# Performance work log

Hardware: AMD Instinct MI355X
Metric: run time of the kernel (lower is better)

## Reference

```python
import jax, jax.numpy as jnp
import numpy as np

EMBED = 2048
HEADS = 16
B, T = 4, 2048


def setup_inputs() -> dict:
    key = jax.random.key(0)
    ks = jax.random.split(key, 8)
    s = 1.0 / np.sqrt(EMBED)
    return {
        "k": jax.random.normal(ks[0], (B, T, EMBED), dtype=jnp.float32),
        "q": jax.random.normal(ks[1], (B, T, EMBED), dtype=jnp.float32),
        "v": jax.random.normal(ks[2], (B, T, EMBED), dtype=jnp.float32),
        "Wk": jax.random.uniform(ks[3], (EMBED, EMBED), jnp.float32, -s, s),
        "Wq": jax.random.uniform(ks[4], (EMBED, EMBED), jnp.float32, -s, s),
        "Wv": jax.random.uniform(ks[5], (EMBED, EMBED), jnp.float32, -s, s),
        "Wo": jax.random.uniform(ks[6], (EMBED, EMBED), jnp.float32, -s, s),
        "bo": jax.random.uniform(ks[7], (EMBED,), jnp.float32, -s, s),
    }


def _split_heads(x):
    b, t, e = x.shape
    # 'b t (h n) -> b h t n'
    return x.reshape(b, t, HEADS, e // HEADS).transpose(0, 2, 1, 3)


def reference(k, q, v, Wk, Wq, Wv, Wo, bo):
    keys = _split_heads(k @ Wk.T)      # [b,h,t,n]
    queries = _split_heads(q @ Wq.T)
    values = _split_heads(v @ Wv.T)
    head_dim = queries.shape[-1]
    scale = 1.0 / jnp.sqrt(jnp.asarray(head_dim, queries.dtype))
    att = jnp.einsum('bhqn,bhkn->bhqk', queries, keys) * scale
    att = jax.nn.softmax(att, axis=-1)
    out = jnp.einsum('bhqk,bhkn->bhqn', att, values)  # [b,h,t,n]
    b, h, t, n = out.shape
    out = out.transpose(0, 2, 1, 3).reshape(b, t, h * n)  # 'b h t n -> b t (h n)'
    return out @ Wo.T + bo
```

## Files before the change

### kernel.cpp

```cpp
#include <hip/hip_runtime.h>


typedef __attribute__((ext_vector_type(4))) float f32x4;
typedef __attribute__((ext_vector_type(2))) float f32x2;
typedef __attribute__((ext_vector_type(8))) __bf16 bf16x8;
typedef __attribute__((ext_vector_type(4))) unsigned int u32x4;
typedef __attribute__((ext_vector_type(2))) unsigned int u32x2;

#define DEVI static __device__ __forceinline__

#define SCQ 0.12751721769f

DEVI unsigned short f2bf(float f) {
  union { float f; unsigned u; } x; x.f = f;
  unsigned u = x.u;
  return (unsigned short)((u + 0x7fffu + ((u >> 16) & 1u)) >> 16);
}
DEVI unsigned int pack2(float lo, float hi) {
  return (unsigned int)f2bf(lo) | ((unsigned int)f2bf(hi) << 16);
}
DEVI u32x4 pack8(const f32x4 a, const f32x4 b) {
  u32x4 r;
  r[0] = pack2(a[0], a[1]); r[1] = pack2(a[2], a[3]);
  r[2] = pack2(b[0], b[1]); r[3] = pack2(b[2], b[3]);
  return r;
}
DEVI void gload16(const unsigned short* g, unsigned short* l) {
  __builtin_amdgcn_global_load_lds(
      (const __attribute__((address_space(1))) unsigned int*)g,
      (__attribute__((address_space(3))) unsigned int*)l, 16, 0, 0);
}

template <int CTRL> DEVI float dppf(float x) {
  return __builtin_bit_cast(float, __builtin_amdgcn_update_dpp(
      __builtin_bit_cast(int, x), __builtin_bit_cast(int, x), CTRL, 0xF, 0xF, true));
}
DEVI float rowmax16(float x) {
  x = fmaxf(x, dppf<0x121>(x));
  x = fmaxf(x, dppf<0x122>(x));
  x = fmaxf(x, dppf<0x124>(x));
  x = fmaxf(x, dppf<0x128>(x));
  return x;
}
DEVI float rowsum16(float x) {
  x += dppf<0x121>(x);
  x += dppf<0x122>(x);
  x += dppf<0x124>(x);
  x += dppf<0x128>(x);
  return x;
}

__global__ __launch_bounds__(256) void convA(
    const float* __restrict__ q, const float* __restrict__ k,
    const float* __restrict__ v, unsigned short* __restrict__ dst)
{
  const int z = blockIdx.z;
  const float* src = z == 0 ? q : (z == 1 ? k : v);
  const float scl = z == 0 ? SCQ : 1.0f;
  unsigned short* d = dst + (size_t)z * 16777216;
  size_t i = ((size_t)blockIdx.x * 256 + threadIdx.x) * 8;
  f32x4 a = *(const f32x4*)(src + i) * scl;
  f32x4 b = *(const f32x4*)(src + i + 4) * scl;
  *(u32x4*)(d + i) = pack8(a, b);
}

__global__ __launch_bounds__(256) void convW(
    const float* __restrict__ w0, const float* __restrict__ w1,
    const float* __restrict__ w2, const float* __restrict__ w3,
    unsigned short* __restrict__ dst)
{
  const int z = blockIdx.z;
  const float* src = z == 0 ? w0 : (z == 1 ? w1 : (z == 2 ? w2 : w3));
  unsigned short* d = dst + (size_t)z * 4194304;
  size_t i = ((size_t)blockIdx.x * 256 + threadIdx.x) * 8;
  f32x4 a = *(const f32x4*)(src + i);
  f32x4 b = *(const f32x4*)(src + i + 4);
  *(u32x4*)(d + i) = pack8(a, b);
}

#define STG1(gp, lp, tile) gload16((gp) + (size_t)(tile) * 32, (lp));
#define LDA8(bufoff) { \
    _Pragma("unroll") for (int m = 0; m < 8; m++) \
      a[m] = *(const bf16x8*)(As + (bufoff) + aoff[m]); }
#define LDB2(bufoff, n0) { \
    b0 = *(const bf16x8*)(Bs + (bufoff) + boff[n0]); \
    b1 = *(const bf16x8*)(Bs + (bufoff) + boff[(n0) + 1]); }
#define MM2(n0) { \
    __builtin_amdgcn_s_setprio(1); \
    _Pragma("unroll") for (int m = 0; m < 8; m++) { \
      acc[m][n0] = __builtin_amdgcn_mfma_f32_16x16x32_bf16(a[m], b0, acc[m][n0], 0, 0, 0); \
      acc[m][(n0) + 1] = __builtin_amdgcn_mfma_f32_16x16x32_bf16(a[m], b1, acc[m][(n0) + 1], 0, 0, 0); \
    } \
    __builtin_amdgcn_s_setprio(0); }
#define BARX() { __builtin_amdgcn_sched_barrier(0); __builtin_amdgcn_s_barrier(); }
#define WVM(n) asm volatile("s_waitcnt vmcnt(" #n ")" ::: "memory");

DEVI void gemm256_bf16(const unsigned short* __restrict__ A,
                       const unsigned short* __restrict__ Bm,
                       unsigned short* As, unsigned short* Bs,
                       int bm, int bn, int tid, f32x4 (&acc)[8][4])
{
  const int lane = tid & 63, w = tid >> 6;
  const int wm = w >> 2, wn = w & 3;
  const int sr = lane >> 2;
  const int sc = (lane & 3) ^ ((sr >> 1) & 3);
  const unsigned short* gA0 = A  + (size_t)(bm * 256 +   0 + w * 16 + sr) * 2048 + sc * 8;
  const unsigned short* gA1 = A  + (size_t)(bm * 256 + 128 + w * 16 + sr) * 2048 + sc * 8;
  const unsigned short* gB0 = Bm + (size_t)(bn * 256 +   0 + w * 16 + sr) * 2048 + sc * 8;
  const unsigned short* gB1 = Bm + (size_t)(bn * 256 + 128 + w * 16 + sr) * 2048 + sc * 8;
  unsigned short* lA00 = As +        (  0 + w * 16) * 32;
  unsigned short* lA01 = As +        (128 + w * 16) * 32;
  unsigned short* lA10 = As + 8192 + (  0 + w * 16) * 32;
  unsigned short* lA11 = As + 8192 + (128 + w * 16) * 32;
  unsigned short* lB00 = Bs +        (  0 + w * 16) * 32;
  unsigned short* lB01 = Bs +        (128 + w * 16) * 32;
  unsigned short* lB10 = Bs + 8192 + (  0 + w * 16) * 32;
  unsigned short* lB11 = Bs + 8192 + (128 + w * 16) * 32;

  const int fr = lane & 15, fk = lane >> 4;
  const int swz = (fk ^ ((fr >> 1) & 3)) << 3;
  int aoff[8], boff[4];
#pragma unroll
  for (int m = 0; m < 8; m++) aoff[m] = (wm * 128 + m * 16 + fr) * 32 + swz;
#pragma unroll
  for (int n = 0; n < 4; n++) boff[n] = (wn * 64 + n * 16 + fr) * 32 + swz;

  bf16x8 a[8], b0, b1;

  STG1(gA0, lA00, 0) STG1(gA1, lA01, 0) STG1(gB0, lB00, 0) STG1(gB1, lB01, 0)
  STG1(gA0, lA10, 1) STG1(gA1, lA11, 1)
  WVM(2) BARX()

  for (int t = 0; t < 62; t += 2) {
    LDA8(0) LDB2(0, 0) STG1(gB0, lB10, t + 1) STG1(gB1, lB11, t + 1)
    BARX() MM2(0) BARX()
    LDB2(0, 2) STG1(gA0, lA00, t + 2) STG1(gA1, lA01, t + 2)
    BARX() MM2(2) WVM(2) BARX()
    LDA8(8192) LDB2(8192, 0) STG1(gB0, lB00, t + 2) STG1(gB1, lB01, t + 2)
    BARX() MM2(0) BARX()
    LDB2(8192, 2) STG1(gA0, lA10, t + 3) STG1(gA1, lA11, t + 3)
    BARX() MM2(2) WVM(2) BARX()
  }
  LDA8(0) LDB2(0, 0) STG1(gB0, lB10, 63) STG1(gB1, lB11, 63)
  BARX() MM2(0) BARX()
  LDB2(0, 2)
  BARX() MM2(2) WVM(0) BARX()
  LDA8(8192) LDB2(8192, 0)
  BARX() MM2(0) BARX()
  LDB2(8192, 2)
  BARX() MM2(2)
}

DEVI int xcd_swz256(int bid) { return ((bid & 7) << 5) | (bid >> 3); }

__global__ __launch_bounds__(512, 2) void qkv_gemm_bf(
    const unsigned short* __restrict__ Abf, const unsigned short* __restrict__ Wbf,
    unsigned short* __restrict__ O0, unsigned short* __restrict__ O1,
    unsigned short* __restrict__ O2)
{
  __shared__ unsigned short As[2 * 256 * 32];
  __shared__ unsigned short Bs[2 * 256 * 32];
  const int z = blockIdx.z;
  const unsigned short* A = Abf + (size_t)z * 16777216;
  const unsigned short* W = Wbf + (size_t)z * 4194304;
  unsigned short* O = z == 0 ? O0 : (z == 1 ? O1 : O2);

  const int tid = threadIdx.x;
  const int lane = tid & 63, w = tid >> 6;
  const int wm = w >> 2, wn = w & 3;
  const int bs = xcd_swz256(blockIdx.x);
  const int bm = bs >> 3, bn = bs & 7;

  f32x4 acc[8][4];
#pragma unroll
  for (int m = 0; m < 8; m++)
#pragma unroll
    for (int n = 0; n < 4; n++) acc[m][n] = (f32x4)(0.0f);

  gemm256_bf16(A, W, As, Bs, bm, bn, tid, acc);

  if (z == 2) {
#pragma unroll
    for (int m = 0; m < 8; m++) {
      int rowg = bm * 256 + wm * 128 + m * 16 + (lane >> 4) * 4;
      int bb = rowg >> 11, t0 = rowg & 2047;
#pragma unroll
      for (int n = 0; n < 4; n++) {
        int col = bn * 256 + wn * 64 + n * 16 + (lane & 15);
        int hh = col >> 7, dd = col & 127;
        u32x2 wv;
        wv[0] = pack2(acc[m][n][0], acc[m][n][1]);
        wv[1] = pack2(acc[m][n][2], acc[m][n][3]);
        *(u32x2*)(O + (((size_t)(bb * 16 + hh) * 128 + dd) << 11) + t0) = wv;
      }
    }
    return;
  }

  const bool evenlane = (lane & 1) == 0;
#pragma unroll
  for (int m = 0; m < 8; m++) {
    int rowg = bm * 256 + wm * 128 + m * 16 + (lane >> 4) * 4;
#pragma unroll
    for (int n = 0; n < 4; n += 2) {
#pragma unroll
      for (int j = 0; j < 4; j++) {
        float v0 = acc[m][n][j], v1 = acc[m][n + 1][j];
        float p0 = __shfl_xor(v0, 1);
        float p1 = __shfl_xor(v1, 1);
        int row = rowg + j;
        int b = row >> 11, t = row & 2047;
        int colbase = bn * 256 + wn * 64;
        int col = evenlane ? (colbase + n * 16 + (lane & 15))
                           : (colbase + (n + 1) * 16 + (lane & 15) - 1);
        unsigned int wv = evenlane ? pack2(v0, p0) : pack2(p1, v1);
        int h = col >> 7, d = col & 127;
        *(unsigned int*)(O + (((size_t)(b * 16 + h) * 2048 + t) << 7) + d) = wv;
      }
    }
  }
}

__global__ __launch_bounds__(512, 2) void out_gemm_bf(
    const unsigned short* __restrict__ Ab, const unsigned short* __restrict__ Wb,
    const float* __restrict__ bias, float* __restrict__ Out)
{
  __shared__ unsigned short As[2 * 256 * 32];
  __shared__ unsigned short Bs[2 * 256 * 32];
  const int tid = threadIdx.x;
  const int lane = tid & 63, w = tid >> 6;
  const int wm = w >> 2, wn = w & 3;
  const int bs = xcd_swz256(blockIdx.x);
  const int bm = bs >> 3, bn = bs & 7;

  f32x4 acc[8][4];
#pragma unroll
  for (int m = 0; m < 8; m++)
#pragma unroll
    for (int n = 0; n < 4; n++) acc[m][n] = (f32x4)(0.0f);

  gemm256_bf16(Ab, Wb, As, Bs, bm, bn, tid, acc);

  float bv[4];
#pragma unroll
  for (int n = 0; n < 4; n++) bv[n] = bias[bn * 256 + wn * 64 + n * 16 + (lane & 15)];
  const bool evenlane = (lane & 1) == 0;
#pragma unroll
  for (int m = 0; m < 8; m++) {
    int rowg = bm * 256 + wm * 128 + m * 16 + (lane >> 4) * 4;
#pragma unroll
    for (int n = 0; n < 4; n += 2) {
#pragma unroll
      for (int j = 0; j < 4; j++) {
        float v0 = acc[m][n][j] + bv[n];
        float v1 = acc[m][n + 1][j] + bv[n + 1];
        float p0 = __shfl_xor(v0, 1);
        float p1 = __shfl_xor(v1, 1);
        int row = rowg + j;
        int colbase = bn * 256 + wn * 64;
        int col = evenlane ? (colbase + n * 16 + (lane & 15))
                           : (colbase + (n + 1) * 16 + (lane & 15) - 1);
        f32x2 wv;
        if (evenlane) { wv[0] = v0; wv[1] = p0; }
        else          { wv[0] = p1; wv[1] = v1; }
        *(f32x2*)(Out + (size_t)row * 2048 + col) = wv;
      }
    }
  }
}

__global__ __launch_bounds__(256) void qkv_gemm(
    const float* __restrict__ A0, const float* __restrict__ A1, const float* __restrict__ A2,
    const float* __restrict__ W0, const float* __restrict__ W1, const float* __restrict__ W2,
    unsigned short* __restrict__ O0, unsigned short* __restrict__ O1, unsigned short* __restrict__ O2)
{
  __shared__ unsigned short As[128 * 32];
  __shared__ unsigned short Bs[128 * 32];
  const int z = blockIdx.z;
  const float* A = z == 0 ? A0 : (z == 1 ? A1 : A2);
  const float* W = z == 0 ? W0 : (z == 1 ? W1 : W2);
  unsigned short* O = z == 0 ? O0 : (z == 1 ? O1 : O2);

  const int tid = threadIdx.x;
  const int lane = tid & 63;
  const int wave = tid >> 6;
  const int wm = wave >> 1, wn = wave & 1;
  const int bm = blockIdx.x >> 4, bn = blockIdx.x & 15;

  const int srow = tid >> 1;
  const int shalf = tid & 1;
  const float* Ap = A + (size_t)(bm * 128 + srow) * 2048 + shalf * 16;
  const float* Wp = W + (size_t)(bn * 128 + srow) * 2048 + shalf * 16;
  const int ssw = (srow >> 1) & 3;
  const int aoff0 = srow * 32 + (((shalf * 2 + 0) ^ ssw) << 3);
  const int aoff1 = srow * 32 + (((shalf * 2 + 1) ^ ssw) << 3);

  const int frow = lane & 15;
  const int fk = lane >> 4;

  f32x4 acc[4][4];
#pragma unroll
  for (int m = 0; m < 4; m++)
#pragma unroll
    for (int n = 0; n < 4; n++) acc[m][n] = (f32x4)(0.0f);

  for (int kk = 0; kk < 2048; kk += 32) {
    f32x4 a0 = *(const f32x4*)(Ap + kk);
    f32x4 a1 = *(const f32x4*)(Ap + kk + 4);
    f32x4 a2 = *(const f32x4*)(Ap + kk + 8);
    f32x4 a3 = *(const f32x4*)(Ap + kk + 12);
    f32x4 b0 = *(const f32x4*)(Wp + kk);
    f32x4 b1 = *(const f32x4*)(Wp + kk + 4);
    f32x4 b2 = *(const f32x4*)(Wp + kk + 8);
    f32x4 b3 = *(const f32x4*)(Wp + kk + 12);
    __syncthreads();
    *(u32x4*)(As + aoff0) = pack8(a0, a1);
    *(u32x4*)(As + aoff1) = pack8(a2, a3);
    *(u32x4*)(Bs + aoff0) = pack8(b0, b1);
    *(u32x4*)(Bs + aoff1) = pack8(b2, b3);
    __syncthreads();
    bf16x8 af[4], bfr[4];
#pragma unroll
    for (int m = 0; m < 4; m++) {
      int r = wm * 64 + m * 16 + frow;
      af[m] = *(const bf16x8*)(As + r * 32 + ((fk ^ ((r >> 1) & 3)) << 3));
    }
#pragma unroll
    for (int n = 0; n < 4; n++) {
      int r = wn * 64 + n * 16 + frow;
      bfr[n] = *(const bf16x8*)(Bs + r * 32 + ((fk ^ ((r >> 1) & 3)) << 3));
    }
#pragma unroll
    for (int m = 0; m < 4; m++)
#pragma unroll
      for (int n = 0; n < 4; n++)
        acc[m][n] = __builtin_amdgcn_mfma_f32_16x16x32_bf16(af[m], bfr[n], acc[m][n], 0, 0, 0);
  }

  if (z == 2) {
#pragma unroll
    for (int m = 0; m < 4; m++) {
      int rowg = bm * 128 + wm * 64 + m * 16 + (lane >> 4) * 4;
      int bb = rowg >> 11, t0 = rowg & 2047;
#pragma unroll
      for (int n = 0; n < 4; n++) {
        int col = bn * 128 + wn * 64 + n * 16 + (lane & 15);
        int hh = col >> 7, dd = col & 127;
        u32x2 wv;
        wv[0] = pack2(acc[m][n][0], acc[m][n][1]);
        wv[1] = pack2(acc[m][n][2], acc[m][n][3]);
        *(u32x2*)(O + (((size_t)(bb * 16 + hh) * 128 + dd) << 11) + t0) = wv;
      }
    }
    return;
  }

  const float scl = (z == 0) ? SCQ : 1.0f;
  const bool evenlane = (lane & 1) == 0;
#pragma unroll
  for (int m = 0; m < 4; m++) {
    int rowg = bm * 128 + wm * 64 + m * 16 + (lane >> 4) * 4;
#pragma unroll
    for (int n = 0; n < 4; n += 2) {
#pragma unroll
      for (int j = 0; j < 4; j++) {
        float v0 = acc[m][n][j] * scl, v1 = acc[m][n + 1][j] * scl;
        float p0 = __shfl_xor(v0, 1);
        float p1 = __shfl_xor(v1, 1);
        int row = rowg + j;
        int b = row >> 11, t = row & 2047;
        int colbase = bn * 128 + wn * 64;
        int col = evenlane ? (colbase + n * 16 + (lane & 15))
                           : (colbase + (n + 1) * 16 + (lane & 15) - 1);
        unsigned int wv = evenlane ? pack2(v0, p0) : pack2(p1, v1);
        int h = col >> 7, d = col & 127;
        *(unsigned int*)(O + (((size_t)(b * 16 + h) * 2048 + t) << 7) + d) = wv;
      }
    }
  }
}

__global__ __launch_bounds__(256, 2) void attn(
    const unsigned short* __restrict__ Qw, const unsigned short* __restrict__ Kw,
    const unsigned short* __restrict__ VwT, unsigned short* __restrict__ attout)
{
  __shared__ unsigned short Ks[2][64 * 128];
  __shared__ unsigned short Vs[2][128 * 64];
  __shared__ unsigned short Ps[128 * 64];

  const int bid = blockIdx.x;
  const int work = ((bid & 7) << 7) | (bid >> 3);
  const int bh = work >> 4;
  const int qtile = work & 15;
  const int b = bh >> 4, h = bh & 15;
  const unsigned short* Qbase = Qw + (size_t)bh * 2048 * 128 + qtile * 128 * 128;
  const unsigned short* Kbase = Kw + (size_t)bh * 2048 * 128;
  const unsigned short* VbaseT = VwT + (size_t)bh * 2048 * 128;
  const int tid = threadIdx.x, lane = tid & 63, w = tid >> 6;
  const int frow = lane & 15, fk = lane >> 4;

  bf16x8 qf[2][4];
#pragma unroll
  for (int m = 0; m < 2; m++)
#pragma unroll
    for (int ks = 0; ks < 4; ks++)
      qf[m][ks] = *(const bf16x8*)(Qbase + (size_t)(w * 32 + m * 16 + frow) * 128 + ks * 32 + fk * 8);

  const int krow_i = lane >> 4;
  const int kslot = lane & 15;
  const int vrow_i = lane >> 3;
  const int vslot = (lane & 7) ^ vrow_i;

  f32x4 o[2][8];
#pragma unroll
  for (int m = 0; m < 2; m++)
#pragma unroll
    for (int n = 0; n < 8; n++) o[m][n] = (f32x4)(0.0f);
  float m_r[2][4], l_p[2][4];
#pragma unroll
  for (int m = 0; m < 2; m++)
#pragma unroll
    for (int j = 0; j < 4; j++) { m_r[m][j] = -INFINITY; l_p[m][j] = 0.f; }
  const float THRL = 11.5f;

  {
#pragma unroll
    for (int i = 0; i < 4; i++) {
      int row = w * 16 + i * 4 + krow_i;
      gload16(Kbase + (size_t)row * 128 + ((kslot ^ (row & 15)) << 3),
              &Ks[0][(w * 16 + i * 4) * 128]);
    }
#pragma unroll
    for (int i = 0; i < 4; i++) {
      int d = w * 32 + i * 8 + vrow_i;
      gload16(VbaseT + (size_t)d * 2048 + vslot * 8,
              &Vs[0][(w * 32 + i * 8) * 64]);
    }
  }

  for (int kt = 0; kt < 32; kt++) {
    const int cur = kt & 1;
    __syncthreads();

    const bool have_next = (kt + 1) < 32;
    if (have_next) {
      const unsigned short* Kt = Kbase + (kt + 1) * 64 * 128;
#pragma unroll
      for (int i = 0; i < 4; i++) {
        int row = w * 16 + i * 4 + krow_i;
        gload16(Kt + (size_t)row * 128 + ((kslot ^ (row & 15)) << 3),
                &Ks[cur ^ 1][(w * 16 + i * 4) * 128]);
      }
#pragma unroll
      for (int i = 0; i < 4; i++) {
        int d = w * 32 + i * 8 + vrow_i;
        gload16(VbaseT + (size_t)d * 2048 + (kt + 1) * 64 + vslot * 8,
                &Vs[cur ^ 1][(w * 32 + i * 8) * 64]);
      }
    }

    f32x4 s[2][4];
    __builtin_amdgcn_s_setprio(1);
#pragma unroll
    for (int n = 0; n < 4; n++) {
      int brow = n * 16 + frow;
      bf16x8 bk = *(const bf16x8*)(&Ks[cur][0] + brow * 128 + ((fk ^ (brow & 15)) << 3));
#pragma unroll
      for (int m = 0; m < 2; m++)
        s[m][n] = __builtin_amdgcn_mfma_f32_16x16x32_bf16(qf[m][0], bk, (f32x4)(0.0f), 0, 0, 0);
    }
#pragma unroll
    for (int ks = 1; ks < 4; ks++) {
#pragma unroll
      for (int n = 0; n < 4; n++) {
        int brow = n * 16 + frow;
        bf16x8 bk = *(const bf16x8*)(&Ks[cur][0] + brow * 128 + (((ks * 4 + fk) ^ (brow & 15)) << 3));
#pragma unroll
        for (int m = 0; m < 2; m++)
          s[m][n] = __builtin_amdgcn_mfma_f32_16x16x32_bf16(qf[m][ks], bk, s[m][n], 0, 0, 0);
      }
    }
    __builtin_amdgcn_s_setprio(0);

#pragma unroll
    for (int m = 0; m < 2; m++) {
#pragma unroll
      for (int j = 0; j < 4; j++) {
        float mx = fmaxf(fmaxf(s[m][0][j], s[m][1][j]), fmaxf(s[m][2][j], s[m][3][j]));
        float mo = m_r[m][j];
        if (!__all(mx - mo <= THRL)) {
          float mnew = fmaxf(mo, rowmax16(mx));
          float f = __builtin_amdgcn_exp2f(mo - mnew);
          m_r[m][j] = mnew;
          l_p[m][j] *= f;
#pragma unroll
          for (int n = 0; n < 8; n++) o[m][n][j] *= f;
        }
        float mm = m_r[m][j];
        float ps = 0.f;
#pragma unroll
        for (int n = 0; n < 4; n++) {
          float p = __builtin_amdgcn_exp2f(s[m][n][j] - mm);
          s[m][n][j] = p;
          ps += p;
        }
        l_p[m][j] += ps;

        int row = w * 32 + m * 16 + (lane >> 4) * 4 + j;
        int swzp = row & 7;
        unsigned prv[4];
#pragma unroll
        for (int n = 0; n < 4; n++) {
          float p = s[m][n][j];
          float ph = dppf<0xB1>(p);
          unsigned pr;
          asm("v_cvt_pk_bf16_f32 %0, %1, %2" : "=v"(pr) : "v"(p), "v"(ph));
          prv[n] = pr;
        }
        if (!(lane & 1)) {
#pragma unroll
          for (int n = 0; n < 4; n++) {
            int col = frow + 16 * n;
            *(unsigned*)((char*)Ps + row * 128 + (((col >> 3) ^ swzp) << 4) + (col & 7) * 2) = prv[n];
          }
        }
      }
    }

    __builtin_amdgcn_s_setprio(1);
#pragma unroll
    for (int ks = 0; ks < 2; ks++) {
      bf16x8 ap[2];
#pragma unroll
      for (int m = 0; m < 2; m++) {
        int arow = w * 32 + m * 16 + frow;
        ap[m] = *(const bf16x8*)((char*)Ps + arow * 128 + (((ks * 4 + fk) ^ (arow & 7)) << 4));
      }
#pragma unroll
      for (int n = 0; n < 8; n++) {
        int vrow = n * 16 + frow;
        bf16x8 bv = *(const bf16x8*)((char*)&Vs[cur][0] + vrow * 128 + (((ks * 4 + fk) ^ (vrow & 7)) << 4));
#pragma unroll
        for (int m = 0; m < 2; m++)
          o[m][n] = __builtin_amdgcn_mfma_f32_16x16x32_bf16(ap[m], bv, o[m][n], 0, 0, 0);
      }
    }
    __builtin_amdgcn_s_setprio(0);
  }

  const bool evenlane = (lane & 1) == 0;
#pragma unroll
  for (int m = 0; m < 2; m++) {
    float inv[4];
#pragma unroll
    for (int j = 0; j < 4; j++) inv[j] = 1.0f / rowsum16(l_p[m][j]);
#pragma unroll
    for (int n = 0; n < 8; n += 2) {
#pragma unroll
      for (int j = 0; j < 4; j++) {
        float v0 = o[m][n][j] * inv[j], v1 = o[m][n + 1][j] * inv[j];
        float p0 = __shfl_xor(v0, 1);
        float p1 = __shfl_xor(v1, 1);
        int tq = qtile * 128 + w * 32 + m * 16 + (lane >> 4) * 4 + j;
        int col = evenlane ? (n * 16 + (lane & 15)) : ((n + 1) * 16 + (lane & 15) - 1);
        unsigned int wv = evenlane ? pack2(v0, p0) : pack2(p1, v1);
        *(unsigned int*)(attout + (size_t)(b * 2048 + tq) * 2048 + h * 128 + col) = wv;
      }
    }
  }
}

__global__ __launch_bounds__(256) void out_gemm(
    const unsigned short* __restrict__ Ab, const float* __restrict__ W,
    const float* __restrict__ bias, float* __restrict__ Out)
{
  __shared__ unsigned short As[128 * 32];
  __shared__ unsigned short Bs[128 * 32];

  const int tid = threadIdx.x;
  const int lane = tid & 63;
  const int wave = tid >> 6;
  const int wm = wave >> 1, wn = wave & 1;
  const int bm = blockIdx.x >> 4, bn = blockIdx.x & 15;

  const int srow = tid >> 1;
  const int shalf = tid & 1;
  const unsigned short* Ap = Ab + (size_t)(bm * 128 + srow) * 2048 + shalf * 16;
  const float* Wp = W + (size_t)(bn * 128 + srow) * 2048 + shalf * 16;
  const int ssw = (srow >> 1) & 3;
  const int aoff0 = srow * 32 + (((shalf * 2 + 0) ^ ssw) << 3);
  const int aoff1 = srow * 32 + (((shalf * 2 + 1) ^ ssw) << 3);

  const int frow = lane & 15;
  const int fk = lane >> 4;

  f32x4 acc[4][4];
#pragma unroll
  for (int m = 0; m < 4; m++)
#pragma unroll
    for (int n = 0; n < 4; n++) acc[m][n] = (f32x4)(0.0f);

  for (int kk = 0; kk < 2048; kk += 32) {
    u32x4 a0 = *(const u32x4*)(Ap + kk);
    u32x4 a1 = *(const u32x4*)(Ap + kk + 8);
    f32x4 b0 = *(const f32x4*)(Wp + kk);
    f32x4 b1 = *(const f32x4*)(Wp + kk + 4);
    f32x4 b2 = *(const f32x4*)(Wp + kk + 8);
    f32x4 b3 = *(const f32x4*)(Wp + kk + 12);
    __syncthreads();
    *(u32x4*)(As + aoff0) = a0;
    *(u32x4*)(As + aoff1) = a1;
    *(u32x4*)(Bs + aoff0) = pack8(b0, b1);
    *(u32x4*)(Bs + aoff1) = pack8(b2, b3);
    __syncthreads();
    bf16x8 af[4], bfr[4];
#pragma unroll
    for (int m = 0; m < 4; m++) {
      int r = wm * 64 + m * 16 + frow;
      af[m] = *(const bf16x8*)(As + r * 32 + ((fk ^ ((r >> 1) & 3)) << 3));
    }
#pragma unroll
    for (int n = 0; n < 4; n++) {
      int r = wn * 64 + n * 16 + frow;
      bfr[n] = *(const bf16x8*)(Bs + r * 32 + ((fk ^ ((r >> 1) & 3)) << 3));
    }
#pragma unroll
    for (int m = 0; m < 4; m++)
#pragma unroll
      for (int n = 0; n < 4; n++)
        acc[m][n] = __builtin_amdgcn_mfma_f32_16x16x32_bf16(af[m], bfr[n], acc[m][n], 0, 0, 0);
  }

  float bv[4];
#pragma unroll
  for (int n = 0; n < 4; n++) bv[n] = bias[bn * 128 + wn * 64 + n * 16 + (lane & 15)];
  const bool evenlane = (lane & 1) == 0;
#pragma unroll
  for (int m = 0; m < 4; m++) {
    int rowg = bm * 128 + wm * 64 + m * 16 + (lane >> 4) * 4;
#pragma unroll
    for (int n = 0; n < 4; n += 2) {
#pragma unroll
      for (int j = 0; j < 4; j++) {
        float v0 = acc[m][n][j] + bv[n];
        float v1 = acc[m][n + 1][j] + bv[n + 1];
        float p0 = __shfl_xor(v0, 1);
        float p1 = __shfl_xor(v1, 1);
        int row = rowg + j;
        int colbase = bn * 128 + wn * 64;
        int col = evenlane ? (colbase + n * 16 + (lane & 15))
                           : (colbase + (n + 1) * 16 + (lane & 15) - 1);
        f32x2 wv;
        if (evenlane) { wv[0] = v0; wv[1] = p0; }
        else          { wv[0] = p1; wv[1] = v1; }
        *(f32x2*)(Out + (size_t)row * 2048 + col) = wv;
      }
    }
  }
}

extern "C" void kernel_launch(void* const* d_in, const int* in_sizes, int n_in,
                              void* d_out, int out_size, void* d_ws, size_t ws_size,
                              hipStream_t stream)
{
  const float* k  = (const float*)d_in[0];
  const float* q  = (const float*)d_in[1];
  const float* v  = (const float*)d_in[2];
  const float* Wk = (const float*)d_in[3];
  const float* Wq = (const float*)d_in[4];
  const float* Wv = (const float*)d_in[5];
  const float* Wo = (const float*)d_in[6];
  const float* bo = (const float*)d_in[7];
  float* out = (float*)d_out;

  const size_t HSZ = (size_t)4 * 16 * 2048 * 128;

  if (ws_size >= (size_t)224 << 20) {
    unsigned short* Abf = (unsigned short*)d_ws;
    unsigned short* Wbf = Abf + 3 * HSZ;
    unsigned short* Qw  = Wbf + 4 * 4194304;
    unsigned short* Kw  = Qw + HSZ;
    unsigned short* Vw  = Kw + HSZ;
    unsigned short* Aw  = Abf;

    convA<<<dim3(8192, 1, 3), 256, 0, stream>>>(q, k, v, Abf);
    convW<<<dim3(2048, 1, 4), 256, 0, stream>>>(Wq, Wk, Wv, Wo, Wbf);
    qkv_gemm_bf<<<dim3(256, 1, 3), 512, 0, stream>>>(Abf, Wbf, Qw, Kw, Vw);
    attn<<<dim3(1024), 256, 0, stream>>>(Qw, Kw, Vw, Aw);
    out_gemm_bf<<<dim3(256), 512, 0, stream>>>(Aw, Wbf + 3 * 4194304, bo, out);
  } else {
    unsigned short* Qw = (unsigned short*)d_ws;
    unsigned short* Kw = Qw + HSZ;
    unsigned short* Vw = Kw + HSZ;
    unsigned short* Aw = Vw + HSZ;
    qkv_gemm<<<dim3(1024, 1, 3), 256, 0, stream>>>(q, k, v, Wq, Wk, Wv, Qw, Kw, Vw);
    attn<<<dim3(1024), 256, 0, stream>>>(Qw, Kw, Vw, Aw);
    out_gemm<<<dim3(1024), 256, 0, stream>>>(Aw, Wo, bo, out);
  }
}
```

Baseline: 534.2 us.

## Deepen bf16 GEMM LDS pipeline to four stages with fewer barriers

The shared 256x256 bf16 GEMM mainloop moves from a double-buffered LDS scheme to a four-stage ring. Global-to-LDS loads now run three K-tiles ahead, and each tile does all four B fragments in one MFMA burst, giving two barriers per tile instead of four. The goal is to hide global load latency better and cut synchronisation overhead. The cost is that LDS per block doubles to 128 KB, which likely leaves room for only one 512-thread block per CU instead of the two the launch bounds ask for. Shared arrays in the fallback kernels are renamed without changing behaviour.

```diff
diff --git a/kernel.cpp b/kernel.cpp
--- a/kernel.cpp
+++ b/kernel.cpp
@@ -78,22 +78,33 @@
   *(u32x4*)(d + i) = pack8(a, b);
 }
 
-#define STG1(gp, lp, tile) gload16((gp) + (size_t)(tile) * 32, (lp));
-#define LDA8(bufoff) { \
+#define LDA8(bi) { \
     _Pragma("unroll") for (int m = 0; m < 8; m++) \
-      a[m] = *(const bf16x8*)(As + (bufoff) + aoff[m]); }
-#define LDB2(bufoff, n0) { \
-    b0 = *(const bf16x8*)(Bs + (bufoff) + boff[n0]); \
-    b1 = *(const bf16x8*)(Bs + (bufoff) + boff[(n0) + 1]); }
-#define MM2(n0) { \
+      a[m] = *(const bf16x8*)(As + (bi) * 8192 + aoff[m]); }
+#define LDB4(bi) { \
+    b0 = *(const bf16x8*)(Bs + (bi) * 8192 + boff[0]); \
+    b1 = *(const bf16x8*)(Bs + (bi) * 8192 + boff[1]); \
+    b2 = *(const bf16x8*)(Bs + (bi) * 8192 + boff[2]); \
+    b3 = *(const bf16x8*)(Bs + (bi) * 8192 + boff[3]); }
+#define STG4(si, tl) { \
+    gload16(gA0 + (size_t)(tl) * 32, lA0 + (si) * 8192); \
+    gload16(gA1 + (size_t)(tl) * 32, lA1 + (si) * 8192); \
+    gload16(gB0 + (size_t)(tl) * 32, lB0 + (si) * 8192); \
+    gload16(gB1 + (size_t)(tl) * 32, lB1 + (si) * 8192); }
+#define MM4() { \
     __builtin_amdgcn_s_setprio(1); \
     _Pragma("unroll") for (int m = 0; m < 8; m++) { \
-      acc[m][n0] = __builtin_amdgcn_mfma_f32_16x16x32_bf16(a[m], b0, acc[m][n0], 0, 0, 0); \
-      acc[m][(n0) + 1] = __builtin_amdgcn_mfma_f32_16x16x32_bf16(a[m], b1, acc[m][(n0) + 1], 0, 0, 0); \
+      acc[m][0] = __builtin_amdgcn_mfma_f32_16x16x32_bf16(a[m], b0, acc[m][0], 0, 0, 0); \
+      acc[m][1] = __builtin_amdgcn_mfma_f32_16x16x32_bf16(a[m], b1, acc[m][1], 0, 0, 0); \
+      acc[m][2] = __builtin_amdgcn_mfma_f32_16x16x32_bf16(a[m], b2, acc[m][2], 0, 0, 0); \
+      acc[m][3] = __builtin_amdgcn_mfma_f32_16x16x32_bf16(a[m], b3, acc[m][3], 0, 0, 0); \
     } \
     __builtin_amdgcn_s_setprio(0); }
 #define BARX() { __builtin_amdgcn_sched_barrier(0); __builtin_amdgcn_s_barrier(); }
 #define WVM(n) asm volatile("s_waitcnt vmcnt(" #n ")" ::: "memory");
+#define PHASE_F(bi, si, tl) \
+    LDA8(bi) LDB4(bi) STG4(si, tl) \
+    BARX() MM4() WVM(8) BARX()
 
 DEVI void gemm256_bf16(const unsigned short* __restrict__ A,
                        const unsigned short* __restrict__ Bm,
@@ -108,14 +119,10 @@
   const unsigned short* gA1 = A  + (size_t)(bm * 256 + 128 + w * 16 + sr) * 2048 + sc * 8;
   const unsigned short* gB0 = Bm + (size_t)(bn * 256 +   0 + w * 16 + sr) * 2048 + sc * 8;
   const unsigned short* gB1 = Bm + (size_t)(bn * 256 + 128 + w * 16 + sr) * 2048 + sc * 8;
-  unsigned short* lA00 = As +        (  0 + w * 16) * 32;
-  unsigned short* lA01 = As +        (128 + w * 16) * 32;
-  unsigned short* lA10 = As + 8192 + (  0 + w * 16) * 32;
-  unsigned short* lA11 = As + 8192 + (128 + w * 16) * 32;
-  unsigned short* lB00 = Bs +        (  0 + w * 16) * 32;
-  unsigned short* lB01 = Bs +        (128 + w * 16) * 32;
-  unsigned short* lB10 = Bs + 8192 + (  0 + w * 16) * 32;
-  unsigned short* lB11 = Bs + 8192 + (128 + w * 16) * 32;
+  unsigned short* lA0 = As + (  0 + w * 16) * 32;
+  unsigned short* lA1 = As + (128 + w * 16) * 32;
+  unsigned short* lB0 = Bs + (  0 + w * 16) * 32;
+  unsigned short* lB1 = Bs + (128 + w * 16) * 32;
 
   const int fr = lane & 15, fk = lane >> 4;
   const int swz = (fk ^ ((fr >> 1) & 3)) << 3;
@@ -125,30 +132,21 @@
 #pragma unroll
   for (int n = 0; n < 4; n++) boff[n] = (wn * 64 + n * 16 + fr) * 32 + swz;
 
-  bf16x8 a[8], b0, b1;
-
-  STG1(gA0, lA00, 0) STG1(gA1, lA01, 0) STG1(gB0, lB00, 0) STG1(gB1, lB01, 0)
-  STG1(gA0, lA10, 1) STG1(gA1, lA11, 1)
-  WVM(2) BARX()
-
-  for (int t = 0; t < 62; t += 2) {
-    LDA8(0) LDB2(0, 0) STG1(gB0, lB10, t + 1) STG1(gB1, lB11, t + 1)
-    BARX() MM2(0) BARX()
-    LDB2(0, 2) STG1(gA0, lA00, t + 2) STG1(gA1, lA01, t + 2)
-    BARX() MM2(2) WVM(2) BARX()
-    LDA8(8192) LDB2(8192, 0) STG1(gB0, lB00, t + 2) STG1(gB1, lB01, t + 2)
-    BARX() MM2(0) BARX()
-    LDB2(8192, 2) STG1(gA0, lA10, t + 3) STG1(gA1, lA11, t + 3)
-    BARX() MM2(2) WVM(2) BARX()
-  }
-  LDA8(0) LDB2(0, 0) STG1(gB0, lB10, 63) STG1(gB1, lB11, 63)
-  BARX() MM2(0) BARX()
-  LDB2(0, 2)
-  BARX() MM2(2) WVM(0) BARX()
-  LDA8(8192) LDB2(8192, 0)
-  BARX() MM2(0) BARX()
-  LDB2(8192, 2)
-  BARX() MM2(2)
+  bf16x8 a[8], b0, b1, b2, b3;
+
+  STG4(0, 0) STG4(1, 1) STG4(2, 2)
+  WVM(8) BARX()
+
+  for (int t = 0; t < 60; t += 4) {
+    PHASE_F(0, 3, t + 3)
+    PHASE_F(1, 0, t + 4)
+    PHASE_F(2, 1, t + 5)
+    PHASE_F(3, 2, t + 6)
+  }
+  PHASE_F(0, 3, 63)
+  LDA8(1) LDB4(1) BARX() MM4() WVM(4) BARX()
+  LDA8(2) LDB4(2) BARX() MM4() WVM(0) BARX()
+  LDA8(3) LDB4(3) BARX() MM4()
 }
 
 DEVI int xcd_swz256(int bid) { return ((bid & 7) << 5) | (bid >> 3); }
@@ -158,8 +156,8 @@
     unsigned short* __restrict__ O0, unsigned short* __restrict__ O1,
     unsigned short* __restrict__ O2)
 {
-  __shared__ unsigned short As[2 * 256 * 32];
-  __shared__ unsigned short Bs[2 * 256 * 32];
+  __shared__ unsigned short As[4 * 256 * 32];
+  __shared__ unsigned short Bs[4 * 256 * 32];
   const int z = blockIdx.z;
   const unsigned short* A = Abf + (size_t)z * 16777216;
   const unsigned short* W = Wbf + (size_t)z * 4194304;
@@ -225,8 +223,8 @@
     const unsigned short* __restrict__ Ab, const unsigned short* __restrict__ Wb,
     const float* __restrict__ bias, float* __restrict__ Out)
 {
-  __shared__ unsigned short As[2 * 256 * 32];
-  __shared__ unsigned short Bs[2 * 256 * 32];
+  __shared__ unsigned short As[4 * 256 * 32];
+  __shared__ unsigned short Bs[4 * 256 * 32];
   const int tid = threadIdx.x;
   const int lane = tid & 63, w = tid >> 6;
   const int wm = w >> 2, wn = w & 3;
@@ -274,8 +272,8 @@
     const float* __restrict__ W0, const float* __restrict__ W1, const float* __restrict__ W2,
     unsigned short* __restrict__ O0, unsigned short* __restrict__ O1, unsigned short* __restrict__ O2)
 {
-  __shared__ unsigned short As[128 * 32];
-  __shared__ unsigned short Bs[128 * 32];
+  __shared__ unsigned short Asf[128 * 32];
+  __shared__ unsigned short Bsf[128 * 32];
   const int z = blockIdx.z;
   const float* A = z == 0 ? A0 : (z == 1 ? A1 : A2);
   const float* W = z == 0 ? W0 : (z == 1 ? W1 : W2);
@@ -314,21 +312,21 @@
     f32x4 b2 = *(const f32x4*)(Wp + kk + 8);
     f32x4 b3 = *(const f32x4*)(Wp + kk + 12);
     __syncthreads();
-    *(u32x4*)(As + aoff0) = pack8(a0, a1);
-    *(u32x4*)(As + aoff1) = pack8(a2, a3);
-    *(u32x4*)(Bs + aoff0) = pack8(b0, b1);
-    *(u32x4*)(Bs + aoff1) = pack8(b2, b3);
+    *(u32x4*)(Asf + aoff0) = pack8(a0, a1);
+    *(u32x4*)(Asf + aoff1) = pack8(a2, a3);
+    *(u32x4*)(Bsf + aoff0) = pack8(b0, b1);
+    *(u32x4*)(Bsf + aoff1) = pack8(b2, b3);
     __syncthreads();
     bf16x8 af[4], bfr[4];
 #pragma unroll
     for (int m = 0; m < 4; m++) {
       int r = wm * 64 + m * 16 + frow;
-      af[m] = *(const bf16x8*)(As + r * 32 + ((fk ^ ((r >> 1) & 3)) << 3));
+      af[m] = *(const bf16x8*)(Asf + r * 32 + ((fk ^ ((r >> 1) & 3)) << 3));
     }
 #pragma unroll
     for (int n = 0; n < 4; n++) {
       int r = wn * 64 + n * 16 + frow;
-      bfr[n] = *(const bf16x8*)(Bs + r * 32 + ((fk ^ ((r >> 1) & 3)) << 3));
+      bfr[n] = *(const bf16x8*)(Bsf + r * 32 + ((fk ^ ((r >> 1) & 3)) << 3));
     }
 #pragma unroll
     for (int m = 0; m < 4; m++)
@@ -574,8 +572,8 @@
     const unsigned short* __restrict__ Ab, const float* __restrict__ W,
     const float* __restrict__ bias, float* __restrict__ Out)
 {
-  __shared__ unsigned short As[128 * 32];
-  __shared__ unsigned short Bs[128 * 32];
+  __shared__ unsigned short Asf[128 * 32];
+  __shared__ unsigned short Bsf[128 * 32];
 
   const int tid = threadIdx.x;
   const int lane = tid & 63;
@@ -608,21 +606,21 @@
     f32x4 b2 = *(const f32x4*)(Wp + kk + 8);
     f32x4 b3 = *(const f32x4*)(Wp + kk + 12);
     __syncthreads();
-    *(u32x4*)(As + aoff0) = a0;
-    *(u32x4*)(As + aoff1) = a1;
-    *(u32x4*)(Bs + aoff0) = pack8(b0, b1);
-    *(u32x4*)(Bs + aoff1) = pack8(b2, b3);
+    *(u32x4*)(Asf + aoff0) = a0;
+    *(u32x4*)(Asf + aoff1) = a1;
+    *(u32x4*)(Bsf + aoff0) = pack8(b0, b1);
+    *(u32x4*)(Bsf + aoff1) = pack8(b2, b3);
     __syncthreads();
     bf16x8 af[4], bfr[4];
 #pragma unroll
     for (int m = 0; m < 4; m++) {
       int r = wm * 64 + m * 16 + frow;
-      af[m] = *(const bf16x8*)(As + r * 32 + ((fk ^ ((r >> 1) & 3)) << 3));
+      af[m] = *(const bf16x8*)(Asf + r * 32 + ((fk ^ ((r >> 1) & 3)) << 3));
     }
 #pragma unroll
     for (int n = 0; n < 4; n++) {
       int r = wn * 64 + n * 16 + frow;
-      bfr[n] = *(const bf16x8*)(Bs + r * 32 + ((fk ^ ((r >> 1) & 3)) << 3));
+      bfr[n] = *(const bf16x8*)(Bsf + r * 32 + ((fk ^ ((r >> 1) & 3)) << 3));
     }
 #pragma unroll
     for (int m = 0; m < 4; m++)
```

After: 542.3 us. Within noise of the previous version (+1.5%).
